# Performance work log

Measured on AMD Instinct MI355X. Metric: run time of the kernel, lower is better.

## Reference

```python
import jax, jax.numpy as jnp
import numpy as np

GROUP = 32  # hadamard group size == MX block size


def _hadamard(n):
    H = np.array([[1.0]], dtype=np.float64)
    while H.shape[0] < n:
        H = np.block([[H, H], [H, -H]])
    return (H * n ** -0.5).astype(np.float32)


def _fp4_e2m1_rne(v):
    # round-to-nearest-even onto {0, 0.5, 1, 1.5, 2, 3, 4, 6} (signed)
    s = jnp.sign(v)
    a = jnp.minimum(jnp.abs(v), 6.0)
    e = jnp.clip(jnp.floor(jnp.log2(jnp.maximum(a, 2.0 ** -10))), 0.0, 2.0)
    step = jnp.exp2(e - 1.0)  # 0.5 / 1 / 2 depending on binade
    return s * jnp.round(a / step) * step  # jnp.round is half-to-even


def _mxfp4_quant_dequant(t):
    # blockwise MXFP4 with power-of-two (E8M0) shared scale per 32 elems
    shp = t.shape
    tb = t.reshape(-1, GROUP)
    amax = jnp.max(jnp.abs(tb), axis=-1, keepdims=True)
    # shared exponent: floor(log2(amax)) - emax_fp4 (=2, since max e2m1 = 6.0)
    scale = jnp.exp2(jnp.floor(jnp.log2(jnp.maximum(amax, 1e-30))) - 2.0)
    scale = jnp.where(amax > 0, scale, 1.0)
    return (_fp4_e2m1_rne(tb / scale) * scale).reshape(shp)


def _rotate(t, hadamard):
    g = hadamard.shape[0]
    return (t.reshape(-1, g) @ hadamard).reshape(t.shape)


def setup_inputs() -> dict:
    key = jax.random.key(0)
    k1, k2, k3 = jax.random.split(key, 3)
    tokens, in_f, out_f = 8192, 4096, 16384
    x = jax.random.normal(k1, (tokens, in_f), dtype=jnp.float32)
    weight = jax.random.normal(k2, (out_f, in_f), dtype=jnp.float32) * (in_f ** -0.5)
    bias = jax.random.normal(k3, (out_f,), dtype=jnp.float32) * 0.01
    hadamard = jnp.asarray(_hadamard(GROUP))
    return {"x": x, "weight": weight, "bias": bias, "hadamard": hadamard}


def reference(x, weight, bias, hadamard) -> jnp.ndarray:
    # pre_forward: dqweight = dequant(mxfp4_quant(hadamard_rotate(weight)))
    w_dq = _mxfp4_quant_dequant(_rotate(weight, hadamard))
    # forward: x -> hadamard rotate -> mxfp4 pseudoquant -> matmul -> +bias
    x_dq = _mxfp4_quant_dequant(_rotate(x, hadamard))
    return x_dq @ w_dq.T + bias
```

## Files before the change

kernel.cpp:

```cpp
#include <hip/hip_runtime.h>
#include <stdint.h>

typedef float v4f  __attribute__((ext_vector_type(4)));
typedef float v16f __attribute__((ext_vector_type(16)));
typedef int   v4i  __attribute__((ext_vector_type(4)));
typedef int   v8i  __attribute__((ext_vector_type(8)));

__device__ __forceinline__ void gload_lds16(const void* g, void* l) {
  __builtin_amdgcn_global_load_lds(
      (const __attribute__((address_space(1))) void*)g,
      (__attribute__((address_space(3))) void*)l, 16, 0, 0);
}
__device__ __forceinline__ void gload_lds4(const void* g, void* l) {
  __builtin_amdgcn_global_load_lds(
      (const __attribute__((address_space(1))) void*)g,
      (__attribute__((address_space(3))) void*)l, 4, 0, 0);
}

__global__ __launch_bounds__(256) void quant_fp4_kernel(
    const float* __restrict__ in, uint32_t* __restrict__ packed,
    uint8_t* __restrict__ scales, int R, int rblkbits) {
  const int bid = blockIdx.x, tid = threadIdx.x;
  const int row = ((bid & ((1 << rblkbits) - 1)) << 3) + (tid & 7);
  const int kb  = ((bid >> rblkbits) << 5) + (tid >> 3);

  float v[32];
  const v4f* p = (const v4f*)(in + (size_t)row * 4096 + kb * 32);
#pragma unroll
  for (int c = 0; c < 8; ++c) {
    v4f t = p[c];
    v[c * 4 + 0] = t[0]; v[c * 4 + 1] = t[1];
    v[c * 4 + 2] = t[2]; v[c * 4 + 3] = t[3];
  }
#pragma unroll
  for (int s = 0; s < 5; ++s) {
    const int h = 1 << s;
#pragma unroll
    for (int k = 0; k < 16; ++k) {
      const int i = ((k >> s) << (s + 1)) | (k & (h - 1));
      float a = v[i], b = v[i + h];
      v[i] = a + b; v[i + h] = a - b;
    }
  }
  const float RS = 0.17677669529663687f;
  float amax = 0.0f;
#pragma unroll
  for (int i = 0; i < 32; ++i) {
    v[i] *= RS;
    amax = fmaxf(amax, fabsf(v[i]));
  }
  int E;
  float rscale;
  if (amax > 0.0f) {
    float am = fmaxf(amax, 1e-30f);
    E = (int)((__float_as_uint(am) >> 23) & 255u) - 127;
    rscale = __uint_as_float((uint32_t)(2 - E + 127) << 23);
  } else { E = 2; rscale = 1.0f; }

  uint32_t dw[4] = {0u, 0u, 0u, 0u};
#pragma unroll
  for (int i = 0; i < 32; ++i) {
    float x = v[i];
    float a = fminf(fabsf(x) * rscale, 6.0f);
    float rstep = a >= 4.0f ? 0.5f : (a >= 2.0f ? 1.0f : 2.0f);
    float step  = a >= 4.0f ? 2.0f : (a >= 2.0f ? 1.0f : 0.5f);
    float q = rintf(a * rstep) * step;
    uint32_t uq = __float_as_uint(q);
    int Eq = (int)(uq >> 23) - 127;
    uint32_t code = (q == 0.0f) ? 0u
                  : (Eq < 0 ? 1u
                            : (((uint32_t)(Eq + 1) << 1) | ((uq >> 22) & 1u)));
    code |= (__float_as_uint(x) >> 31) << 3;
    dw[i >> 3] |= code << (4 * (i & 7));
  }
  uint4 o; o.x = dw[0]; o.y = dw[1]; o.z = dw[2]; o.w = dw[3];
  *(uint4*)(packed + ((size_t)kb * R + row) * 4) = o;

  const int kt = kb >> 3, hik = kb & 1, ks = (kb >> 1) & 3;
  scales[(size_t)((kt * 2 + hik) * R + row) * 4 + ks] = (uint8_t)(E - 2 + 127);
}

#define MFMA4(a, b, c, sa, sb) \
  __builtin_amdgcn_mfma_scale_f32_32x32x64_f8f6f4((a), (b), (c), 4, 4, 0, (sa), 0, (sb))
#define PAD8(x) __builtin_shufflevector((x), (x), 0, 1, 2, 3, -1, -1, -1, -1)
#define BARRIER { asm volatile("" ::: "memory"); __builtin_amdgcn_s_barrier(); asm volatile("" ::: "memory"); }
#define SB0 __builtin_amdgcn_sched_barrier(0)
#define LGKM0 { asm volatile("s_waitcnt lgkmcnt(0)" ::: "memory"); SB0; }
#define VMW(n)  asm volatile("s_waitcnt vmcnt(" #n ")" ::: "memory")

__global__ __launch_bounds__(512, 2) void gemm_fp4_2x(
    const uint8_t* __restrict__ Apk, const uint8_t* __restrict__ Bpk,
    const uint32_t* __restrict__ Asc, const uint32_t* __restrict__ Bsc,
    const float* __restrict__ bias, float* __restrict__ C) {
  const int N = 16384;
  __shared__ uint8_t lds[139264];

  const int tid = threadIdx.x, lane = tid & 63, wv = tid >> 6;
  const int wm = wv >> 2, wn = wv & 3;
  const int hi = lane >> 5, r32 = lane & 31;

  const int bid = blockIdx.x;
  const int xcd = bid & 7, idx = bid >> 3, st = idx >> 5;
  const int mT = ((st & 3) * 8 + (idx & 7)) * 256;
  const int nT = (xcd * 8 + (st >> 2) * 4 + ((idx >> 3) & 3)) * 256;

  const int sOp = wv >> 2;
  const int sR2 = (wv >> 1) & 1;
  const int s0  = 2 * (wv & 1);
  const uint8_t* opBase = sOp ? Bpk : Apk;
  const size_t RB = sOp ? (size_t)16384 * 16 : (size_t)8192 * 16;
  const int T0 = sOp ? nT : mT;
  const size_t gOff0 = (size_t)(T0 + (s0 + 0) * 64 + lane) * 16;
  const size_t gOff1 = (size_t)(T0 + (s0 + 1) * 64 + lane) * 16;
  const int dOff0 = sOp * 32768 + sR2 * 4096 + (s0 + 0) * 1024 + lane * 16;
  const int dOff1 = sOp * 32768 + sR2 * 4096 + (s0 + 1) * 1024 + lane * 16;

  auto STG_OPS = [&](int kt, int a, int bb) {
    const uint8_t* g0 = opBase + (size_t)(kt * 8 + a + sR2) * RB;
    uint8_t* l = &lds[bb * 65536 + a * 4096];
    gload_lds16(g0 + gOff0, l + dOff0);
    gload_lds16(g0 + gOff1, l + dOff1);
  };

  const uint32_t* scBase = sOp ? Bsc : Asc;
  const int Rrows = sOp ? 16384 : 8192;
  auto STG_SC = [&](int kt, int bb) {
    const uint32_t* g = scBase + (size_t)(kt * 2 + sR2) * Rrows + T0;
    uint8_t* l = &lds[131072 + bb * 4096 + sOp * 2048 + sR2 * 1024];
    gload_lds4(g + (s0 + 0) * 64 + lane, l + (s0 + 0) * 256 + lane * 4);
    gload_lds4(g + (s0 + 1) * 64 + lane, l + (s0 + 1) * 256 + lane * 4);
  };

  const int aRd0 = hi * 4096 + (wm * 128 + r32) * 16;
  const int aRd1 = aRd0 + 65536;
  const int bRd0 = 32768 + hi * 4096 + (wn * 64 + r32) * 16;
  const int bRd1 = bRd0 + 65536;
  const int aSc0 = 131072 + hi * 1024 + (wm * 128 + r32) * 4;
  const int aSc1 = aSc0 + 4096;
  const int bSc0 = 131072 + 2048 + hi * 1024 + (wn * 64 + r32) * 4;
  const int bSc1 = bSc0 + 4096;

  v16f acc[4][2] = {};
  v4i fA0[4], fB0[2], fA1[4], fB1[2];
  uint32_t saD[4], sbD[2];

#define LDF(FA, FB, ARD, BRD, j) { \
    _Pragma("unroll") for (int mf = 0; mf < 4; ++mf) \
      FA[mf] = *(const v4i*)&lds[(ARD) + (j) * 8192 + mf * 512]; \
    _Pragma("unroll") for (int nf = 0; nf < 2; ++nf) \
      FB[nf] = *(const v4i*)&lds[(BRD) + (j) * 8192 + nf * 512]; }

#define SCRD(ASC, BSC) { \
    _Pragma("unroll") for (int mf = 0; mf < 4; ++mf) \
      saD[mf] = *(const uint32_t*)&lds[(ASC) + mf * 128]; \
    _Pragma("unroll") for (int nf = 0; nf < 2; ++nf) \
      sbD[nf] = *(const uint32_t*)&lds[(BSC) + nf * 128]; }

#define MM8(FA, FB, j) { \
    __builtin_amdgcn_s_setprio(1); \
    _Pragma("unroll") for (int mf = 0; mf < 4; ++mf) \
    _Pragma("unroll") for (int nf = 0; nf < 2; ++nf) \
      acc[mf][nf] = MFMA4(PAD8(FA[mf]), PAD8(FB[nf]), acc[mf][nf], \
                          (int)((saD[mf] >> (8 * (j))) & 255u), \
                          (int)((sbD[nf] >> (8 * (j))) & 255u)); \
    __builtin_amdgcn_s_setprio(0); }

#define TILE2(bb, t, ARD, BRD, ASC, BSC, ob) { \
     \
    SCRD(ASC, BSC); \
    LDF(fA0, fB0, ARD, BRD, 0); SB0; LDF(fA1, fB1, ARD, BRD, 1); \
    STG_OPS((t) + 1, 4, ob); STG_OPS((t) + 1, 6, ob); SB0; \
    BARRIER; LGKM0; \
    MM8(fA0, fB0, 0); MM8(fA1, fB1, 1); \
    BARRIER; \
     \
    LDF(fA0, fB0, ARD, BRD, 2); SB0; LDF(fA1, fB1, ARD, BRD, 3); \
    STG_OPS((t) + 2, 0, bb); STG_OPS((t) + 2, 2, bb); STG_SC((t) + 2, bb); SB0; \
    BARRIER; LGKM0; \
    MM8(fA0, fB0, 2); MM8(fA1, fB1, 3); \
    VMW(6); BARRIER; }

  STG_OPS(0, 0, 0); STG_OPS(0, 2, 0); STG_OPS(0, 4, 0); STG_OPS(0, 6, 0);
  STG_SC(0, 0);
  STG_OPS(1, 0, 1); STG_OPS(1, 2, 1);
  STG_SC(1, 1);
  VMW(6);
  BARRIER;

#pragma unroll 1
  for (int i = 0; i < 7; ++i) {
    const int t0 = 2 * i;
    TILE2(0, t0,     aRd0, bRd0, aSc0, bSc0, 1);
    TILE2(1, t0 + 1, aRd1, bRd1, aSc1, bSc1, 0);
  }

  SCRD(aSc0, bSc0);
  LDF(fA0, fB0, aRd0, bRd0, 0); SB0; LDF(fA1, fB1, aRd0, bRd0, 1);
  STG_OPS(15, 4, 1); STG_OPS(15, 6, 1); SB0;
  BARRIER; LGKM0;
  MM8(fA0, fB0, 0); MM8(fA1, fB1, 1);
  BARRIER;
  LDF(fA0, fB0, aRd0, bRd0, 2); SB0; LDF(fA1, fB1, aRd0, bRd0, 3);
  BARRIER; LGKM0;
  MM8(fA0, fB0, 2); MM8(fA1, fB1, 3);
  VMW(0); BARRIER;

  SCRD(aSc1, bSc1);
  LDF(fA0, fB0, aRd1, bRd1, 0); SB0; LDF(fA1, fB1, aRd1, bRd1, 1);
  LGKM0;
  MM8(fA0, fB0, 0); MM8(fA1, fB1, 1);
  LDF(fA0, fB0, aRd1, bRd1, 2); SB0; LDF(fA1, fB1, aRd1, bRd1, 3);
  LGKM0;
  MM8(fA0, fB0, 2); MM8(fA1, fB1, 3);

#pragma unroll
  for (int nf = 0; nf < 2; ++nf) {
    const int col = nT + wn * 64 + nf * 32 + r32;
    const float bv = bias[col];
#pragma unroll
    for (int mf = 0; mf < 4; ++mf) {
      const int rbase = mT + wm * 128 + mf * 32 + 4 * hi;
#pragma unroll
      for (int q = 0; q < 16; ++q) {
        const int rowl = (q & 3) + 8 * (q >> 2);
        C[(size_t)(rbase + rowl) * N + col] = acc[mf][nf][q] + bv;
      }
    }
  }
}

extern "C" void kernel_launch(void* const* d_in, const int* in_sizes, int n_in,
                              void* d_out, int out_size, void* d_ws, size_t ws_size,
                              hipStream_t stream) {
  const float* x    = (const float*)d_in[0];
  const float* w    = (const float*)d_in[1];
  const float* bias = (const float*)d_in[2];
  float* out = (float*)d_out;

  uint8_t* x_pk = (uint8_t*)d_ws;
  uint8_t* w_pk = x_pk + (size_t)16 * 1024 * 1024;
  uint8_t* x_sc = w_pk + (size_t)32 * 1024 * 1024;
  uint8_t* w_sc = x_sc + (size_t)1  * 1024 * 1024;

  quant_fp4_kernel<<<4096, 256, 0, stream>>>(x, (uint32_t*)x_pk, x_sc, 8192, 10);
  quant_fp4_kernel<<<8192, 256, 0, stream>>>(w, (uint32_t*)w_pk, w_sc, 16384, 11);

  gemm_fp4_2x<<<2048, dim3(512), 0, stream>>>(
      x_pk, w_pk, (const uint32_t*)x_sc, (const uint32_t*)w_sc, bias, out);
}
```

Before: 453.4 us.

## Load B fragments directly into registers and ring-buffer A in LDS

The GEMM now streams only the A operand (and its scales) through a three-slot LDS ring. B fragments and B scales are loaded straight from global memory into registers, double-buffered across k-tiles. This cuts LDS traffic and barrier count and shrinks the LDS footprint. The cost is more registers, and B reads from global are no longer shared across the waves that read the same columns. The two quantization launches are also merged into a single kernel to save one launch.

```diff
diff --git a/kernel.cpp b/kernel.cpp
--- a/kernel.cpp
+++ b/kernel.cpp
@@ -4,7 +4,6 @@
 typedef float v4f  __attribute__((ext_vector_type(4)));
 typedef float v16f __attribute__((ext_vector_type(16)));
 typedef int   v4i  __attribute__((ext_vector_type(4)));
-typedef int   v8i  __attribute__((ext_vector_type(8)));
 
 __device__ __forceinline__ void gload_lds16(const void* g, void* l) {
   __builtin_amdgcn_global_load_lds(
@@ -17,10 +16,16 @@
       (__attribute__((address_space(3))) void*)l, 4, 0, 0);
 }
 
-__global__ __launch_bounds__(256) void quant_fp4_kernel(
-    const float* __restrict__ in, uint32_t* __restrict__ packed,
-    uint8_t* __restrict__ scales, int R, int rblkbits) {
-  const int bid = blockIdx.x, tid = threadIdx.x;
+__global__ __launch_bounds__(256) void quant_fp4_all(
+    const float* __restrict__ x, const float* __restrict__ w,
+    uint32_t* __restrict__ xpk, uint32_t* __restrict__ wpk,
+    uint8_t* __restrict__ xsc, uint8_t* __restrict__ wsc) {
+  int bid = blockIdx.x;
+  const float* in; uint32_t* packed; uint8_t* scales; int R, rblkbits;
+  if (bid < 4096) { in = x; packed = xpk; scales = xsc; R = 8192;  rblkbits = 10; }
+  else { bid -= 4096; in = w; packed = wpk; scales = wsc; R = 16384; rblkbits = 11; }
+
+  const int tid = threadIdx.x;
   const int row = ((bid & ((1 << rblkbits) - 1)) << 3) + (tid & 7);
   const int kb  = ((bid >> rblkbits) << 5) + (tid >> 3);
 
@@ -60,8 +65,8 @@
   uint32_t dw[4] = {0u, 0u, 0u, 0u};
 #pragma unroll
   for (int i = 0; i < 32; ++i) {
-    float x = v[i];
-    float a = fminf(fabsf(x) * rscale, 6.0f);
+    float xx = v[i];
+    float a = fminf(fabsf(xx) * rscale, 6.0f);
     float rstep = a >= 4.0f ? 0.5f : (a >= 2.0f ? 1.0f : 2.0f);
     float step  = a >= 4.0f ? 2.0f : (a >= 2.0f ? 1.0f : 0.5f);
     float q = rintf(a * rstep) * step;
@@ -70,7 +75,7 @@
     uint32_t code = (q == 0.0f) ? 0u
                   : (Eq < 0 ? 1u
                             : (((uint32_t)(Eq + 1) << 1) | ((uq >> 22) & 1u)));
-    code |= (__float_as_uint(x) >> 31) << 3;
+    code |= (__float_as_uint(xx) >> 31) << 3;
     dw[i >> 3] |= code << (4 * (i & 7));
   }
   uint4 o; o.x = dw[0]; o.y = dw[1]; o.z = dw[2]; o.w = dw[3];
@@ -88,12 +93,14 @@
 #define LGKM0 { asm volatile("s_waitcnt lgkmcnt(0)" ::: "memory"); SB0; }
 #define VMW(n)  asm volatile("s_waitcnt vmcnt(" #n ")" ::: "memory")
 
-__global__ __launch_bounds__(512, 2) void gemm_fp4_2x(
+#define RING_SZ 34816
+
+__global__ __launch_bounds__(512, 2) void gemm_fp4_breg(
     const uint8_t* __restrict__ Apk, const uint8_t* __restrict__ Bpk,
     const uint32_t* __restrict__ Asc, const uint32_t* __restrict__ Bsc,
     const float* __restrict__ bias, float* __restrict__ C) {
   const int N = 16384;
-  __shared__ uint8_t lds[139264];
+  __shared__ uint8_t lds[3 * RING_SZ];
 
   const int tid = threadIdx.x, lane = tid & 63, wv = tid >> 6;
   const int wm = wv >> 2, wn = wv & 3;
@@ -104,114 +111,84 @@
   const int mT = ((st & 3) * 8 + (idx & 7)) * 256;
   const int nT = (xcd * 8 + (st >> 2) * 4 + ((idx >> 3) & 3)) * 256;
 
-  const int sOp = wv >> 2;
-  const int sR2 = (wv >> 1) & 1;
-  const int s0  = 2 * (wv & 1);
-  const uint8_t* opBase = sOp ? Bpk : Apk;
-  const size_t RB = sOp ? (size_t)16384 * 16 : (size_t)8192 * 16;
-  const int T0 = sOp ? nT : mT;
-  const size_t gOff0 = (size_t)(T0 + (s0 + 0) * 64 + lane) * 16;
-  const size_t gOff1 = (size_t)(T0 + (s0 + 1) * 64 + lane) * 16;
-  const int dOff0 = sOp * 32768 + sR2 * 4096 + (s0 + 0) * 1024 + lane * 16;
-  const int dOff1 = sOp * 32768 + sR2 * 4096 + (s0 + 1) * 1024 + lane * 16;
-
-  auto STG_OPS = [&](int kt, int a, int bb) {
-    const uint8_t* g0 = opBase + (size_t)(kt * 8 + a + sR2) * RB;
-    uint8_t* l = &lds[bb * 65536 + a * 4096];
-    gload_lds16(g0 + gOff0, l + dOff0);
-    gload_lds16(g0 + gOff1, l + dOff1);
-  };
-
-  const uint32_t* scBase = sOp ? Bsc : Asc;
-  const int Rrows = sOp ? 16384 : 8192;
-  auto STG_SC = [&](int kt, int bb) {
-    const uint32_t* g = scBase + (size_t)(kt * 2 + sR2) * Rrows + T0;
-    uint8_t* l = &lds[131072 + bb * 4096 + sOp * 2048 + sR2 * 1024];
-    gload_lds4(g + (s0 + 0) * 64 + lane, l + (s0 + 0) * 256 + lane * 4);
-    gload_lds4(g + (s0 + 1) * 64 + lane, l + (s0 + 1) * 256 + lane * 4);
-  };
-
-  const int aRd0 = hi * 4096 + (wm * 128 + r32) * 16;
-  const int aRd1 = aRd0 + 65536;
-  const int bRd0 = 32768 + hi * 4096 + (wn * 64 + r32) * 16;
-  const int bRd1 = bRd0 + 65536;
-  const int aSc0 = 131072 + hi * 1024 + (wm * 128 + r32) * 4;
-  const int aSc1 = aSc0 + 4096;
-  const int bSc0 = 131072 + 2048 + hi * 1024 + (wn * 64 + r32) * 4;
-  const int bSc1 = bSc0 + 4096;
+  size_t aSrc[4]; int aDst[4];
+#pragma unroll
+  for (int q = 0; q < 4; ++q) {
+    const int c = q * 512 + tid;
+    aSrc[q] = (size_t)(c >> 8) * 131072 + ((size_t)mT + (c & 255)) * 16;
+    aDst[q] = c * 16;
+  }
+  const int ascFix = ((tid >> 8) & 1) * 8192 + mT + (tid & 255);
+  const int ascDst = 32768 + (tid & 511) * 4;
+
+#define ASTG(tt, RG) { \
+  _Pragma("unroll") for (int q = 0; q < 4; ++q) \
+    gload_lds16(Apk + (size_t)(tt) * 1048576 + aSrc[q], &lds[(RG) + aDst[q]]); \
+  gload_lds4(Asc + (size_t)(tt) * 16384 + ascFix, &lds[(RG) + ascDst]); }
+
+  const size_t bColOff = ((size_t)nT + wn * 64 + r32) * 16;
+  const uint32_t* bScBase = Bsc + nT + wn * 64 + r32;
+
+#define BLOAD(FB, SB, tt) { \
+  _Pragma("unroll") for (int j = 0; j < 4; ++j) \
+  _Pragma("unroll") for (int nf = 0; nf < 2; ++nf) \
+    FB[j * 2 + nf] = *(const v4i*)(Bpk + \
+        (size_t)((tt) * 8 + 2 * j + hi) * 262144 + bColOff + nf * 512); \
+  _Pragma("unroll") for (int nf = 0; nf < 2; ++nf) \
+    SB[nf] = bScBase[(size_t)((tt) * 2 + hi) * 16384 + nf * 32]; }
+
+  const int aFixed = hi * 4096 + (wm * 128 + r32) * 16;
+  const int sFixed = hi * 1024 + (wm * 128 + r32) * 4;
 
   v16f acc[4][2] = {};
-  v4i fA0[4], fB0[2], fA1[4], fB1[2];
-  uint32_t saD[4], sbD[2];
-
-#define LDF(FA, FB, ARD, BRD, j) { \
+  v4i fB0[8], fB1[8];
+  uint32_t sb0[2], sb1[2];
+
+#define COMPUTE(RG, FB, SB) { \
+  const int aA = (RG) + aFixed; \
+  const int sA = (RG) + 32768 + sFixed; \
+  uint32_t saD[4]; \
+  _Pragma("unroll") for (int mf = 0; mf < 4; ++mf) \
+    saD[mf] = *(const uint32_t*)&lds[sA + mf * 128]; \
+  _Pragma("unroll") for (int j = 0; j < 4; ++j) { \
+    v4i fa[4]; \
     _Pragma("unroll") for (int mf = 0; mf < 4; ++mf) \
-      FA[mf] = *(const v4i*)&lds[(ARD) + (j) * 8192 + mf * 512]; \
-    _Pragma("unroll") for (int nf = 0; nf < 2; ++nf) \
-      FB[nf] = *(const v4i*)&lds[(BRD) + (j) * 8192 + nf * 512]; }
-
-#define SCRD(ASC, BSC) { \
-    _Pragma("unroll") for (int mf = 0; mf < 4; ++mf) \
-      saD[mf] = *(const uint32_t*)&lds[(ASC) + mf * 128]; \
-    _Pragma("unroll") for (int nf = 0; nf < 2; ++nf) \
-      sbD[nf] = *(const uint32_t*)&lds[(BSC) + nf * 128]; }
-
-#define MM8(FA, FB, j) { \
+      fa[mf] = *(const v4i*)&lds[aA + j * 8192 + mf * 512]; \
+    LGKM0; \
     __builtin_amdgcn_s_setprio(1); \
     _Pragma("unroll") for (int mf = 0; mf < 4; ++mf) \
     _Pragma("unroll") for (int nf = 0; nf < 2; ++nf) \
-      acc[mf][nf] = MFMA4(PAD8(FA[mf]), PAD8(FB[nf]), acc[mf][nf], \
-                          (int)((saD[mf] >> (8 * (j))) & 255u), \
-                          (int)((sbD[nf] >> (8 * (j))) & 255u)); \
-    __builtin_amdgcn_s_setprio(0); }
-
-#define TILE2(bb, t, ARD, BRD, ASC, BSC, ob) { \
-     \
-    SCRD(ASC, BSC); \
-    LDF(fA0, fB0, ARD, BRD, 0); SB0; LDF(fA1, fB1, ARD, BRD, 1); \
-    STG_OPS((t) + 1, 4, ob); STG_OPS((t) + 1, 6, ob); SB0; \
-    BARRIER; LGKM0; \
-    MM8(fA0, fB0, 0); MM8(fA1, fB1, 1); \
-    BARRIER; \
-     \
-    LDF(fA0, fB0, ARD, BRD, 2); SB0; LDF(fA1, fB1, ARD, BRD, 3); \
-    STG_OPS((t) + 2, 0, bb); STG_OPS((t) + 2, 2, bb); STG_SC((t) + 2, bb); SB0; \
-    BARRIER; LGKM0; \
-    MM8(fA0, fB0, 2); MM8(fA1, fB1, 3); \
-    VMW(6); BARRIER; }
-
-  STG_OPS(0, 0, 0); STG_OPS(0, 2, 0); STG_OPS(0, 4, 0); STG_OPS(0, 6, 0);
-  STG_SC(0, 0);
-  STG_OPS(1, 0, 1); STG_OPS(1, 2, 1);
-  STG_SC(1, 1);
-  VMW(6);
+      acc[mf][nf] = MFMA4(PAD8(fa[mf]), PAD8(FB[j * 2 + nf]), acc[mf][nf], \
+                          (int)((saD[mf] >> (8 * j)) & 255u), \
+                          (int)((SB[nf] >> (8 * j)) & 255u)); \
+    __builtin_amdgcn_s_setprio(0); \
+  } }
+
+  ASTG(0, 0); ASTG(1, RING_SZ); BLOAD(fB0, sb0, 0);
+  VMW(0);
   BARRIER;
 
+  int rC = 0;
+  int rS = 2 * RING_SZ;
 #pragma unroll 1
   for (int i = 0; i < 7; ++i) {
     const int t0 = 2 * i;
-    TILE2(0, t0,     aRd0, bRd0, aSc0, bSc0, 1);
-    TILE2(1, t0 + 1, aRd1, bRd1, aSc1, bSc1, 0);
-  }
-
-  SCRD(aSc0, bSc0);
-  LDF(fA0, fB0, aRd0, bRd0, 0); SB0; LDF(fA1, fB1, aRd0, bRd0, 1);
-  STG_OPS(15, 4, 1); STG_OPS(15, 6, 1); SB0;
-  BARRIER; LGKM0;
-  MM8(fA0, fB0, 0); MM8(fA1, fB1, 1);
-  BARRIER;
-  LDF(fA0, fB0, aRd0, bRd0, 2); SB0; LDF(fA1, fB1, aRd0, bRd0, 3);
-  BARRIER; LGKM0;
-  MM8(fA0, fB0, 2); MM8(fA1, fB1, 3);
+    BLOAD(fB1, sb1, t0 + 1); ASTG(t0 + 2, rS); SB0;
+    COMPUTE(rC, fB0, sb0);
+    VMW(5); BARRIER;
+    rC = (rC == 2 * RING_SZ) ? 0 : rC + RING_SZ;
+    rS = (rS == 2 * RING_SZ) ? 0 : rS + RING_SZ;
+    BLOAD(fB0, sb0, t0 + 2); ASTG(t0 + 3, rS); SB0;
+    COMPUTE(rC, fB1, sb1);
+    VMW(5); BARRIER;
+    rC = (rC == 2 * RING_SZ) ? 0 : rC + RING_SZ;
+    rS = (rS == 2 * RING_SZ) ? 0 : rS + RING_SZ;
+  }
+  BLOAD(fB1, sb1, 15); SB0;
+  COMPUTE(rC, fB0, sb0);
   VMW(0); BARRIER;
-
-  SCRD(aSc1, bSc1);
-  LDF(fA0, fB0, aRd1, bRd1, 0); SB0; LDF(fA1, fB1, aRd1, bRd1, 1);
-  LGKM0;
-  MM8(fA0, fB0, 0); MM8(fA1, fB1, 1);
-  LDF(fA0, fB0, aRd1, bRd1, 2); SB0; LDF(fA1, fB1, aRd1, bRd1, 3);
-  LGKM0;
-  MM8(fA0, fB0, 2); MM8(fA1, fB1, 3);
+  rC = (rC == 2 * RING_SZ) ? 0 : rC + RING_SZ;
+  COMPUTE(rC, fB1, sb1);
 
 #pragma unroll
   for (int nf = 0; nf < 2; ++nf) {
@@ -242,9 +219,9 @@
   uint8_t* x_sc = w_pk + (size_t)32 * 1024 * 1024;
   uint8_t* w_sc = x_sc + (size_t)1  * 1024 * 1024;
 
-  quant_fp4_kernel<<<4096, 256, 0, stream>>>(x, (uint32_t*)x_pk, x_sc, 8192, 10);
-  quant_fp4_kernel<<<8192, 256, 0, stream>>>(w, (uint32_t*)w_pk, w_sc, 16384, 11);
-
-  gemm_fp4_2x<<<2048, dim3(512), 0, stream>>>(
+  quant_fp4_all<<<12288, 256, 0, stream>>>(
+      x, w, (uint32_t*)x_pk, (uint32_t*)w_pk, x_sc, w_sc);
+
+  gemm_fp4_breg<<<2048, dim3(512), 0, stream>>>(
       x_pk, w_pk, (const uint32_t*)x_sc, (const uint32_t*)w_sc, bias, out);
 }
```

New measurement: 486.6 us. +7.3%, slower.
